# Performance work log

Hardware: AMD Instinct MI355X
Metric: run time of the kernel (lower is better)

## Reference

```python
import jax, jax.numpy as jnp
import numpy as np


def _eta(pos, conj):
    # e[0] = pos[:,1::2] repeated into even/odd cols; e[1] = (+/-)pos[:,0::2] likewise
    c = jnp.repeat(pos[:, 1::2], 2, axis=1)
    s = jnp.repeat(pos[:, 0::2], 2, axis=1)
    return jnp.stack([c, s if conj else -s])  # [2, N, d]


def setup_inputs() -> dict:
    key = jax.random.key(0)
    ks = jax.random.split(key, 8)
    B, N, d, H = 8, 4096, 128, 4
    s = 0.02
    return {
        "x": jax.random.normal(ks[0], (B, N, d), jnp.float32),
        "pos": jax.random.normal(ks[1], (N, d), jnp.float32),
        "W_lt": jax.random.normal(ks[2], (d, d), jnp.float32) * s,
        "W_phi": jax.random.normal(ks[3], (d * H, d), jnp.float32) * s,
        "b_phi": jnp.zeros((d * H,), jnp.float32),
        "W_c1": jax.random.normal(ks[4], (H, H), jnp.float32) * s,
        "b_c1": jnp.zeros((H,), jnp.float32),
        "W_c2": jax.random.normal(ks[5], (1, H), jnp.float32) * s,
        "b_c2": jnp.zeros((1,), jnp.float32),
        "ln_g": jnp.ones((d,), jnp.float32),
        "ln_b": jnp.zeros((d,), jnp.float32),
        "W_f1": jax.random.normal(ks[6], (d, d), jnp.float32) * s,
        "b_f1": jnp.zeros((d,), jnp.float32),
        "W_f2": jax.random.normal(ks[7], (d, d), jnp.float32) * s,
        "b_f2": jnp.zeros((d,), jnp.float32),
    }


def reference(x, pos, W_lt, W_phi, b_phi, W_c1, b_c1, W_c2, b_c2,
              ln_g, ln_b, W_f1, b_f1, W_f2, b_f2):
    B, N, d = x.shape
    H = W_phi.shape[0] // d
    x = x @ W_lt.T                                   # linear_trans (no bias)
    e = _eta(pos, False)                             # [2,N,d]
    xe = x[None] * e[:, None]                        # [2,B,N,d]
    # A = ones(N,N) - I  =>  A @ v == sum over nodes minus self
    f = xe.sum(axis=2, keepdims=True) - xe           # [2,B,N,d]
    f_norm = jnp.sqrt(f[0] ** 2 + f[1] ** 2)         # [B,N,d]
    phi = ((x + pos[None]) @ W_phi.T + b_phi).reshape(B, N, H, d)
    # ReLU1(|f| - phi): relu(min(1, f_norm - phi))
    res = jax.nn.relu(jnp.minimum(1.0, f_norm[:, :, None, :] - phi))  # [B,N,H,d]
    ce = _eta(pos, True)
    fec = f[0] * ce[0][None] - f[1] * ce[1][None]    # [B,N,d]
    rfe = res * fec[:, :, None, :]                   # [B,N,H,d]
    # inverse transform: (1/N) * (M @ A) with A symmetric => sum-minus-self over node dim
    inv = (rfe.sum(axis=1, keepdims=True) - rfe) / N  # [B,N,H,d]
    t = inv.transpose(0, 1, 3, 2)                    # [B,N,d,H]
    comb = (jax.nn.relu(t @ W_c1.T + b_c1) @ W_c2.T + b_c2)[..., 0]  # [B,N,d]
    m = x + comb
    mu = m.mean(-1, keepdims=True)
    var = ((m - mu) ** 2).mean(-1, keepdims=True)
    mn = (m - mu) * jax.lax.rsqrt(var + 1e-6) * ln_g + ln_b
    return jax.nn.relu(mn @ W_f1.T + b_f1) @ W_f2.T + b_f2
```

## Files before the change

kernel.cpp:

```cpp
#include <hip/hip_runtime.h>
#include <hip/hip_bf16.h>


#define DEV __device__ __forceinline__

typedef __attribute__((ext_vector_type(8))) short bf16x8;
typedef __attribute__((ext_vector_type(4))) float f32x4;

constexpr int Bb = 8, Nn = 4096;
constexpr int BN = Bb * Nn;
constexpr int LDP = 136;

union U8 { ushort u[8]; uint4 v; };

static DEV ushort f2bf(float f) {
    __hip_bfloat16 h = __float2bfloat16(f);
    return *reinterpret_cast<ushort*>(&h);
}

template <int MODE>
__global__ __launch_bounds__(256) void k_mfma_gemm(
    const void* __restrict__ Xv, const float* __restrict__ W,
    const float* __restrict__ bias, const float* __restrict__ pos,
    float* __restrict__ outF, ushort* __restrict__ outB)
{
    __shared__ __align__(16) ushort xs[64 * LDP];
    __shared__ __align__(16) ushort wsl[128 * LDP];
    const int t = threadIdx.x;
    const int row0 = blockIdx.x * 64;
    const int jt = (MODE == 1) ? blockIdx.y : 0;

    {
        const float* X = (const float*)Xv;
        #pragma unroll
        for (int i = 0; i < 4; ++i) {
            int e = t + i * 256, r = e >> 4, c = (e & 15) * 8;
            const float* p = X + (size_t)(row0 + r) * 128 + c;
            float4 a = *reinterpret_cast<const float4*>(p);
            float4 b = *reinterpret_cast<const float4*>(p + 4);
            if (MODE == 1) {
                int n = (row0 + r) & (Nn - 1);
                const float* q = pos + (size_t)n * 128 + c;
                float4 pa = *reinterpret_cast<const float4*>(q);
                float4 pb = *reinterpret_cast<const float4*>(q + 4);
                a.x += pa.x; a.y += pa.y; a.z += pa.z; a.w += pa.w;
                b.x += pb.x; b.y += pb.y; b.z += pb.z; b.w += pb.w;
            }
            U8 u;
            u.u[0] = f2bf(a.x); u.u[1] = f2bf(a.y); u.u[2] = f2bf(a.z); u.u[3] = f2bf(a.w);
            u.u[4] = f2bf(b.x); u.u[5] = f2bf(b.y); u.u[6] = f2bf(b.z); u.u[7] = f2bf(b.w);
            *reinterpret_cast<uint4*>(xs + r * LDP + c) = u.v;
        }
    }
    {
        const float* Wt = W + (size_t)jt * 128 * 128;
        #pragma unroll
        for (int i = 0; i < 8; ++i) {
            int e = t + i * 256, r = e >> 4, c = (e & 15) * 8;
            const float* p = Wt + (size_t)r * 128 + c;
            float4 a = *reinterpret_cast<const float4*>(p);
            float4 b = *reinterpret_cast<const float4*>(p + 4);
            U8 u;
            u.u[0] = f2bf(a.x); u.u[1] = f2bf(a.y); u.u[2] = f2bf(a.z); u.u[3] = f2bf(a.w);
            u.u[4] = f2bf(b.x); u.u[5] = f2bf(b.y); u.u[6] = f2bf(b.z); u.u[7] = f2bf(b.w);
            *reinterpret_cast<uint4*>(wsl + r * LDP + c) = u.v;
        }
    }
    __syncthreads();

    const int w = t >> 6, l = t & 63;
    const int lr = l & 15;
    const int lk = (l >> 4) * 8;

    f32x4 acc[8];
    #pragma unroll
    for (int cf = 0; cf < 8; ++cf) acc[cf] = f32x4{0.f, 0.f, 0.f, 0.f};

    #pragma unroll
    for (int ks = 0; ks < 4; ++ks) {
        bf16x8 a = *reinterpret_cast<const bf16x8*>(xs + (w * 16 + lr) * LDP + ks * 32 + lk);
        #pragma unroll
        for (int cf = 0; cf < 8; ++cf) {
            bf16x8 b = *reinterpret_cast<const bf16x8*>(wsl + (cf * 16 + lr) * LDP + ks * 32 + lk);
            acc[cf] = __builtin_amdgcn_mfma_f32_16x16x32_bf16(a, b, acc[cf], 0, 0, 0);
        }
    }

    #pragma unroll
    for (int cf = 0; cf < 8; ++cf) {
        int col = cf * 16 + lr;
        float bv = (MODE >= 1) ? bias[jt * 128 + col] : 0.f;
        #pragma unroll
        for (int reg = 0; reg < 4; ++reg) {
            int r = row0 + w * 16 + (l >> 4) * 4 + reg;
            float o = acc[cf][reg] + bv;
            if (MODE == 1) outB[(size_t)r * 512 + jt * 128 + col] = f2bf(o);
            else           outF[(size_t)r * 128 + col] = o;
        }
    }
}

__global__ __launch_bounds__(256) void k_reduceS(
    const float* __restrict__ x1, const float* __restrict__ pos,
    float* __restrict__ S0, float* __restrict__ S1)
{
    int b = blockIdx.x >> 6, c64 = blockIdx.x & 63;
    int d = threadIdx.x & 127, g = threadIdx.x >> 7;
    float a0 = 0.f, a1 = 0.f;
    #pragma unroll 4
    for (int i = 0; i < 32; ++i) {
        int n = c64 * 64 + i * 2 + g;
        float xv = x1[((size_t)b * Nn + n) * 128 + d];
        float2 p2 = *reinterpret_cast<const float2*>(pos + (size_t)n * 128 + (d & ~1));
        a0 += xv * p2.y;
        a1 += xv * p2.x;
    }
    __shared__ float red[2][2][128];
    red[g][0][d] = a0; red[g][1][d] = a1;
    __syncthreads();
    if (g == 0) {
        atomicAdd(&S0[b * 128 + d], a0 + red[1][0][d]);
        atomicAdd(&S1[b * 128 + d], a1 + red[1][1][d]);
    }
}

__global__ __launch_bounds__(256) void k_reduceT(
    const float* __restrict__ x1, const ushort* __restrict__ phi,
    const float* __restrict__ pos, const float* __restrict__ S0,
    const float* __restrict__ S1, float* __restrict__ T)
{
    int b = blockIdx.x >> 6, c64 = blockIdx.x & 63;
    int d = threadIdx.x & 127, g = threadIdx.x >> 7;
    float S0v = S0[b * 128 + d], S1v = S1[b * 128 + d];
    float acc[4] = {0.f, 0.f, 0.f, 0.f};
    #pragma unroll 2
    for (int i = 0; i < 32; ++i) {
        int n = c64 * 64 + i * 2 + g;
        size_t r = (size_t)b * Nn + n;
        float xv = x1[r * 128 + d];
        float2 p2 = *reinterpret_cast<const float2*>(pos + (size_t)n * 128 + (d & ~1));
        float cc = p2.y, ss = p2.x;
        float f0 = S0v - xv * cc;
        float f1 = xv * ss - S1v;
        float fn = sqrtf(f0 * f0 + f1 * f1);
        float fec = f0 * cc - f1 * ss;
        #pragma unroll
        for (int h = 0; h < 4; ++h) {
            float ph = __bfloat162float(*reinterpret_cast<const __hip_bfloat16*>(phi + r * 512 + h * 128 + d));
            float res = fmaxf(0.f, fminf(1.f, fn - ph));
            acc[h] += res * fec;
        }
    }
    __shared__ float red[2][4][128];
    #pragma unroll
    for (int h = 0; h < 4; ++h) red[g][h][d] = acc[h];
    __syncthreads();
    if (g == 0) {
        #pragma unroll
        for (int h = 0; h < 4; ++h)
            atomicAdd(&T[(b * 4 + h) * 128 + d], acc[h] + red[1][h][d]);
    }
}

__global__ __launch_bounds__(256) void k_comb_ln(
    const float* __restrict__ x1, const ushort* __restrict__ phi,
    const float* __restrict__ pos, const float* __restrict__ S0,
    const float* __restrict__ S1, const float* __restrict__ T,
    const float* __restrict__ Wc1, const float* __restrict__ bc1,
    const float* __restrict__ Wc2, const float* __restrict__ bc2,
    const float* __restrict__ lng, const float* __restrict__ lnb,
    ushort* __restrict__ mnB)
{
    int w = threadIdx.x >> 6, l = threadIdx.x & 63;
    int rrow = blockIdx.x * 4 + w;
    int b = rrow >> 12;
    int n = rrow & 4095;

    float m[2];
    #pragma unroll
    for (int q = 0; q < 2; ++q) {
        int d = l + q * 64;
        float xv = x1[(size_t)rrow * 128 + d];
        float2 p2 = *reinterpret_cast<const float2*>(pos + (size_t)n * 128 + (d & ~1));
        float cc = p2.y, ss = p2.x;
        float f0 = S0[b * 128 + d] - xv * cc;
        float f1 = xv * ss - S1[b * 128 + d];
        float fn = sqrtf(f0 * f0 + f1 * f1);
        float fec = f0 * cc - f1 * ss;
        float inv[4];
        #pragma unroll
        for (int h = 0; h < 4; ++h) {
            float ph = __bfloat162float(*reinterpret_cast<const __hip_bfloat16*>(phi + (size_t)rrow * 512 + h * 128 + d));
            float res = fmaxf(0.f, fminf(1.f, fn - ph));
            float rfe = res * fec;
            inv[h] = (T[(b * 4 + h) * 128 + d] - rfe) * (1.f / (float)Nn);
        }
        float comb = bc2[0];
        #pragma unroll
        for (int h = 0; h < 4; ++h) {
            float u = bc1[h];
            #pragma unroll
            for (int h2 = 0; h2 < 4; ++h2) u += Wc1[h * 4 + h2] * inv[h2];
            comb += fmaxf(u, 0.f) * Wc2[h];
        }
        m[q] = xv + comb;
    }

    float s = m[0] + m[1];
    #pragma unroll
    for (int off = 32; off; off >>= 1) s += __shfl_xor(s, off);
    float mu = s * (1.f / 128.f);
    float d0 = m[0] - mu, d1 = m[1] - mu;
    float v = d0 * d0 + d1 * d1;
    #pragma unroll
    for (int off = 32; off; off >>= 1) v += __shfl_xor(v, off);
    float rstd = rsqrtf(v * (1.f / 128.f) + 1e-6f);
    mnB[(size_t)rrow * 128 + l]      = f2bf(d0 * rstd * lng[l] + lnb[l]);
    mnB[(size_t)rrow * 128 + l + 64] = f2bf(d1 * rstd * lng[l + 64] + lnb[l + 64]);
}

__global__ __launch_bounds__(256) void k_ffn(
    const ushort* __restrict__ mnB, const float* __restrict__ Wf1,
    const float* __restrict__ bf1, const float* __restrict__ Wf2,
    const float* __restrict__ bf2, float* __restrict__ out)
{
    __shared__ __align__(16) ushort xs[64 * LDP];
    __shared__ __align__(16) ushort wsl[128 * LDP];
    const int t = threadIdx.x;
    const int row0 = blockIdx.x * 64;

    #pragma unroll
    for (int i = 0; i < 4; ++i) {
        int e = t + i * 256, r = e >> 4, c = (e & 15) * 8;
        uint4 v = *reinterpret_cast<const uint4*>(mnB + (size_t)(row0 + r) * 128 + c);
        *reinterpret_cast<uint4*>(xs + r * LDP + c) = v;
    }
    #pragma unroll
    for (int i = 0; i < 8; ++i) {
        int e = t + i * 256, r = e >> 4, c = (e & 15) * 8;
        const float* p = Wf1 + (size_t)r * 128 + c;
        float4 a = *reinterpret_cast<const float4*>(p);
        float4 b = *reinterpret_cast<const float4*>(p + 4);
        U8 u;
        u.u[0] = f2bf(a.x); u.u[1] = f2bf(a.y); u.u[2] = f2bf(a.z); u.u[3] = f2bf(a.w);
        u.u[4] = f2bf(b.x); u.u[5] = f2bf(b.y); u.u[6] = f2bf(b.z); u.u[7] = f2bf(b.w);
        *reinterpret_cast<uint4*>(wsl + r * LDP + c) = u.v;
    }
    __syncthreads();

    const int w = t >> 6, l = t & 63;
    const int lr = l & 15;
    const int lk = (l >> 4) * 8;

    f32x4 acc[8];
    #pragma unroll
    for (int cf = 0; cf < 8; ++cf) acc[cf] = f32x4{0.f, 0.f, 0.f, 0.f};
    #pragma unroll
    for (int ks = 0; ks < 4; ++ks) {
        bf16x8 a = *reinterpret_cast<const bf16x8*>(xs + (w * 16 + lr) * LDP + ks * 32 + lk);
        #pragma unroll
        for (int cf = 0; cf < 8; ++cf) {
            bf16x8 b = *reinterpret_cast<const bf16x8*>(wsl + (cf * 16 + lr) * LDP + ks * 32 + lk);
            acc[cf] = __builtin_amdgcn_mfma_f32_16x16x32_bf16(a, b, acc[cf], 0, 0, 0);
        }
    }

    __syncthreads();

    #pragma unroll
    for (int cf = 0; cf < 8; ++cf) {
        int col = cf * 16 + lr;
        float bv = bf1[col];
        #pragma unroll
        for (int reg = 0; reg < 4; ++reg) {
            int rl = w * 16 + (l >> 4) * 4 + reg;
            xs[rl * LDP + col] = f2bf(fmaxf(acc[cf][reg] + bv, 0.f));
        }
    }
    #pragma unroll
    for (int i = 0; i < 8; ++i) {
        int e = t + i * 256, r = e >> 4, c = (e & 15) * 8;
        const float* p = Wf2 + (size_t)r * 128 + c;
        float4 a = *reinterpret_cast<const float4*>(p);
        float4 b = *reinterpret_cast<const float4*>(p + 4);
        U8 u;
        u.u[0] = f2bf(a.x); u.u[1] = f2bf(a.y); u.u[2] = f2bf(a.z); u.u[3] = f2bf(a.w);
        u.u[4] = f2bf(b.x); u.u[5] = f2bf(b.y); u.u[6] = f2bf(b.z); u.u[7] = f2bf(b.w);
        *reinterpret_cast<uint4*>(wsl + r * LDP + c) = u.v;
    }
    __syncthreads();

    #pragma unroll
    for (int cf = 0; cf < 8; ++cf) acc[cf] = f32x4{0.f, 0.f, 0.f, 0.f};
    #pragma unroll
    for (int ks = 0; ks < 4; ++ks) {
        bf16x8 a = *reinterpret_cast<const bf16x8*>(xs + (w * 16 + lr) * LDP + ks * 32 + lk);
        #pragma unroll
        for (int cf = 0; cf < 8; ++cf) {
            bf16x8 b = *reinterpret_cast<const bf16x8*>(wsl + (cf * 16 + lr) * LDP + ks * 32 + lk);
            acc[cf] = __builtin_amdgcn_mfma_f32_16x16x32_bf16(a, b, acc[cf], 0, 0, 0);
        }
    }

    #pragma unroll
    for (int cf = 0; cf < 8; ++cf) {
        int col = cf * 16 + lr;
        float bv = bf2[col];
        #pragma unroll
        for (int reg = 0; reg < 4; ++reg) {
            int r = row0 + w * 16 + (l >> 4) * 4 + reg;
            out[(size_t)r * 128 + col] = acc[cf][reg] + bv;
        }
    }
}

extern "C" void kernel_launch(void* const* d_in, const int* in_sizes, int n_in,
                              void* d_out, int out_size, void* d_ws, size_t ws_size,
                              hipStream_t stream)
{
    const float* x    = (const float*)d_in[0];
    const float* pos  = (const float*)d_in[1];
    const float* Wlt  = (const float*)d_in[2];
    const float* Wphi = (const float*)d_in[3];
    const float* bphi = (const float*)d_in[4];
    const float* Wc1  = (const float*)d_in[5];
    const float* bc1  = (const float*)d_in[6];
    const float* Wc2  = (const float*)d_in[7];
    const float* bc2  = (const float*)d_in[8];
    const float* lng  = (const float*)d_in[9];
    const float* lnb  = (const float*)d_in[10];
    const float* Wf1  = (const float*)d_in[11];
    const float* bf1  = (const float*)d_in[12];
    const float* Wf2  = (const float*)d_in[13];
    const float* bf2  = (const float*)d_in[14];

    float* ws = (float*)d_ws;
    float* x1 = ws;
    ushort* mnB = (ushort*)(ws + 4194304);
    float* S0 = ws + 8388608;
    float* S1 = S0 + 1024;
    float* T  = S1 + 1024;
    ushort* phi = (ushort*)(ws + 8394752);
    float* out = (float*)d_out;

    hipMemsetAsync(S0, 0, (1024 + 1024 + 4096) * sizeof(float), stream);

    k_mfma_gemm<0><<<dim3(BN / 64), 256, 0, stream>>>(x, Wlt, nullptr, nullptr, x1, nullptr);
    k_reduceS<<<dim3(512), 256, 0, stream>>>(x1, pos, S0, S1);
    k_mfma_gemm<1><<<dim3(BN / 64, 4), 256, 0, stream>>>(x1, Wphi, bphi, pos, nullptr, phi);
    k_reduceT<<<dim3(512), 256, 0, stream>>>(x1, phi, pos, S0, S1, T);
    k_comb_ln<<<dim3(BN / 4), 256, 0, stream>>>(x1, phi, pos, S0, S1, T,
                                                Wc1, bc1, Wc2, bc2, lng, lnb, mnB);
    k_ffn<<<dim3(BN / 64), 256, 0, stream>>>(mnB, Wf1, bf1, Wf2, bf2, out);
}
```

Before: 83.39 us.

## Fuse S and T reductions into GEMM epilogues with deterministic partial sums

Computes the per-batch S0/S1 reductions in the epilogue of the first GEMM, and the T reduction in the epilogue of the phi GEMM, using registers and shared-memory partials. This removes the separate k_reduceS and k_reduceT passes that re-read x1 and phi from global memory. Per-block partials go to workspace and are summed by small finalize kernels, which also removes the memset and the global atomics. In exchange the GEMM epilogues get heavier, the phi GEMM re-reads x1 for each of its four column tiles, and T is now built from unrounded fp32 phi instead of the stored bf16 values.

```diff
diff --git a/kernel.cpp b/kernel.cpp
--- a/kernel.cpp
+++ b/kernel.cpp
@@ -20,18 +20,22 @@
 
 template <int MODE>
 __global__ __launch_bounds__(256) void k_mfma_gemm(
-    const void* __restrict__ Xv, const float* __restrict__ W,
+    const float* __restrict__ X, const float* __restrict__ W,
     const float* __restrict__ bias, const float* __restrict__ pos,
-    float* __restrict__ outF, ushort* __restrict__ outB)
+    float* __restrict__ outF, ushort* __restrict__ outB,
+    float* __restrict__ PS, float* __restrict__ PT,
+    const float* __restrict__ S0c, const float* __restrict__ S1c)
 {
     __shared__ __align__(16) ushort xs[64 * LDP];
     __shared__ __align__(16) ushort wsl[128 * LDP];
+    __shared__ float red[256];
     const int t = threadIdx.x;
     const int row0 = blockIdx.x * 64;
     const int jt = (MODE == 1) ? blockIdx.y : 0;
 
+    red[t] = 0.f;
+
     {
-        const float* X = (const float*)Xv;
         #pragma unroll
         for (int i = 0; i < 4; ++i) {
             int e = t + i * 256, r = e >> 4, c = (e & 15) * 8;
@@ -86,80 +90,81 @@
         }
     }
 
+    const int bidb = row0 >> 12;
     #pragma unroll
     for (int cf = 0; cf < 8; ++cf) {
         int col = cf * 16 + lr;
-        float bv = (MODE >= 1) ? bias[jt * 128 + col] : 0.f;
-        #pragma unroll
-        for (int reg = 0; reg < 4; ++reg) {
-            int r = row0 + w * 16 + (l >> 4) * 4 + reg;
-            float o = acc[cf][reg] + bv;
-            if (MODE == 1) outB[(size_t)r * 512 + jt * 128 + col] = f2bf(o);
-            else           outF[(size_t)r * 128 + col] = o;
-        }
-    }
-}
-
-__global__ __launch_bounds__(256) void k_reduceS(
-    const float* __restrict__ x1, const float* __restrict__ pos,
-    float* __restrict__ S0, float* __restrict__ S1)
-{
-    int b = blockIdx.x >> 6, c64 = blockIdx.x & 63;
-    int d = threadIdx.x & 127, g = threadIdx.x >> 7;
-    float a0 = 0.f, a1 = 0.f;
-    #pragma unroll 4
-    for (int i = 0; i < 32; ++i) {
-        int n = c64 * 64 + i * 2 + g;
-        float xv = x1[((size_t)b * Nn + n) * 128 + d];
-        float2 p2 = *reinterpret_cast<const float2*>(pos + (size_t)n * 128 + (d & ~1));
-        a0 += xv * p2.y;
-        a1 += xv * p2.x;
-    }
-    __shared__ float red[2][2][128];
-    red[g][0][d] = a0; red[g][1][d] = a1;
-    __syncthreads();
-    if (g == 0) {
-        atomicAdd(&S0[b * 128 + d], a0 + red[1][0][d]);
-        atomicAdd(&S1[b * 128 + d], a1 + red[1][1][d]);
-    }
-}
-
-__global__ __launch_bounds__(256) void k_reduceT(
-    const float* __restrict__ x1, const ushort* __restrict__ phi,
-    const float* __restrict__ pos, const float* __restrict__ S0,
-    const float* __restrict__ S1, float* __restrict__ T)
-{
-    int b = blockIdx.x >> 6, c64 = blockIdx.x & 63;
-    int d = threadIdx.x & 127, g = threadIdx.x >> 7;
-    float S0v = S0[b * 128 + d], S1v = S1[b * 128 + d];
-    float acc[4] = {0.f, 0.f, 0.f, 0.f};
-    #pragma unroll 2
-    for (int i = 0; i < 32; ++i) {
-        int n = c64 * 64 + i * 2 + g;
-        size_t r = (size_t)b * Nn + n;
-        float xv = x1[r * 128 + d];
-        float2 p2 = *reinterpret_cast<const float2*>(pos + (size_t)n * 128 + (d & ~1));
-        float cc = p2.y, ss = p2.x;
-        float f0 = S0v - xv * cc;
-        float f1 = xv * ss - S1v;
-        float fn = sqrtf(f0 * f0 + f1 * f1);
-        float fec = f0 * cc - f1 * ss;
-        #pragma unroll
-        for (int h = 0; h < 4; ++h) {
-            float ph = __bfloat162float(*reinterpret_cast<const __hip_bfloat16*>(phi + r * 512 + h * 128 + d));
-            float res = fmaxf(0.f, fminf(1.f, fn - ph));
-            acc[h] += res * fec;
-        }
-    }
-    __shared__ float red[2][4][128];
-    #pragma unroll
-    for (int h = 0; h < 4; ++h) red[g][h][d] = acc[h];
-    __syncthreads();
-    if (g == 0) {
-        #pragma unroll
-        for (int h = 0; h < 4; ++h)
-            atomicAdd(&T[(b * 4 + h) * 128 + d], acc[h] + red[1][h][d]);
-    }
+        if (MODE == 0) {
+            float s0c = 0.f, s1c = 0.f;
+            #pragma unroll
+            for (int reg = 0; reg < 4; ++reg) {
+                int r = row0 + w * 16 + (l >> 4) * 4 + reg;
+                float o = acc[cf][reg];
+                outF[(size_t)r * 128 + col] = o;
+                int n = r & (Nn - 1);
+                float2 p2 = *reinterpret_cast<const float2*>(pos + (size_t)n * 128 + (col & ~1));
+                s0c += o * p2.y;
+                s1c += o * p2.x;
+            }
+            s0c += __shfl_xor(s0c, 16); s0c += __shfl_xor(s0c, 32);
+            s1c += __shfl_xor(s1c, 16); s1c += __shfl_xor(s1c, 32);
+            if ((l >> 4) == 0) {
+                atomicAdd(&red[col], s0c);
+                atomicAdd(&red[128 + col], s1c);
+            }
+        } else {
+            float S0v = S0c[bidb * 128 + col];
+            float S1v = S1c[bidb * 128 + col];
+            float bv = bias[jt * 128 + col];
+            float tp = 0.f;
+            #pragma unroll
+            for (int reg = 0; reg < 4; ++reg) {
+                int r = row0 + w * 16 + (l >> 4) * 4 + reg;
+                float o = acc[cf][reg] + bv;
+                outB[(size_t)r * 512 + jt * 128 + col] = f2bf(o);
+                int n = r & (Nn - 1);
+                float xv = X[(size_t)r * 128 + col];
+                float2 p2 = *reinterpret_cast<const float2*>(pos + (size_t)n * 128 + (col & ~1));
+                float cc = p2.y, ss = p2.x;
+                float f0 = S0v - xv * cc;
+                float f1 = xv * ss - S1v;
+                float fn = sqrtf(f0 * f0 + f1 * f1);
+                float fec = f0 * cc - f1 * ss;
+                float res = fmaxf(0.f, fminf(1.f, fn - o));
+                tp += res * fec;
+            }
+            tp += __shfl_xor(tp, 16); tp += __shfl_xor(tp, 32);
+            if ((l >> 4) == 0) atomicAdd(&red[col], tp);
+        }
+    }
+    __syncthreads();
+    if (MODE == 0) {
+        PS[(size_t)blockIdx.x * 256 + t] = red[t];
+    } else if (t < 128) {
+        PT[((size_t)blockIdx.x * 4 + jt) * 128 + t] = red[t];
+    }
+}
+
+__global__ __launch_bounds__(256) void k_finS(
+    const float* __restrict__ PS, float* __restrict__ S0, float* __restrict__ S1)
+{
+    int b = blockIdx.x, t = threadIdx.x;
+    float s = 0.f;
+    #pragma unroll 8
+    for (int c = 0; c < 64; ++c) s += PS[(size_t)(b * 64 + c) * 256 + t];
+    if (t < 128) S0[b * 128 + t] = s;
+    else         S1[b * 128 + (t - 128)] = s;
+}
+
+__global__ __launch_bounds__(256) void k_finT(
+    const float* __restrict__ PT, float* __restrict__ T)
+{
+    int idx = blockIdx.x * 256 + threadIdx.x;
+    int b = idx >> 9, lo = idx & 511;
+    float s = 0.f;
+    #pragma unroll 8
+    for (int c = 0; c < 64; ++c) s += PT[(size_t)b * 32768 + c * 512 + lo];
+    T[idx] = s;
 }
 
 __global__ __launch_bounds__(256) void k_comb_ln(
@@ -335,20 +340,22 @@
     const float* bf2  = (const float*)d_in[14];
 
     float* ws = (float*)d_ws;
-    float* x1 = ws;
+    float* x1   = ws;
     ushort* mnB = (ushort*)(ws + 4194304);
-    float* S0 = ws + 8388608;
-    float* S1 = S0 + 1024;
-    float* T  = S1 + 1024;
-    ushort* phi = (ushort*)(ws + 8394752);
-    float* out = (float*)d_out;
-
-    hipMemsetAsync(S0, 0, (1024 + 1024 + 4096) * sizeof(float), stream);
-
-    k_mfma_gemm<0><<<dim3(BN / 64), 256, 0, stream>>>(x, Wlt, nullptr, nullptr, x1, nullptr);
-    k_reduceS<<<dim3(512), 256, 0, stream>>>(x1, pos, S0, S1);
-    k_mfma_gemm<1><<<dim3(BN / 64, 4), 256, 0, stream>>>(x1, Wphi, bphi, pos, nullptr, phi);
-    k_reduceT<<<dim3(512), 256, 0, stream>>>(x1, phi, pos, S0, S1, T);
+    float* S0   = ws + 6291456;
+    float* S1   = S0 + 1024;
+    float* T    = S1 + 1024;
+    float* PS   = T + 4096;
+    float* PT   = PS + 131072;
+    ushort* phi = (ushort*)(PT + 262144);
+    float* out  = (float*)d_out;
+
+    k_mfma_gemm<0><<<dim3(BN / 64), 256, 0, stream>>>(
+        x, Wlt, nullptr, pos, x1, nullptr, PS, nullptr, nullptr, nullptr);
+    k_finS<<<dim3(Bb), 256, 0, stream>>>(PS, S0, S1);
+    k_mfma_gemm<1><<<dim3(BN / 64, 4), 256, 0, stream>>>(
+        x1, Wphi, bphi, pos, nullptr, phi, nullptr, PT, S0, S1);
+    k_finT<<<dim3(16), 256, 0, stream>>>(PT, T);
     k_comb_ln<<<dim3(BN / 4), 256, 0, stream>>>(x1, phi, pos, S0, S1, T,
                                                 Wc1, bc1, Wc2, bc2, lng, lnb, mnB);
     k_ffn<<<dim3(BN / 64), 256, 0, stream>>>(mnB, Wf1, bf1, Wf2, bf2, out);
```

New measurement: 84.75 us. About the same (+1.6%).
